# Performance work log

Measured on AMD Instinct MI355X. Metric: run time of the kernel, lower is better.

Reference implementation:

```python
import jax, jax.numpy as jnp
import numpy as np

B, S, H, NH, HD, I = 2, 1024, 4096, 32, 128, 11008
EPS = 1e-6
THETA = 10000.0


def _rmsnorm(x, w):
    v = jnp.mean(x * x, axis=-1, keepdims=True)
    return x * jax.lax.rsqrt(v + EPS) * w


def _quant(x):
    # per-tensor symmetric int8 quantization (scale already folded upstream)
    return jnp.clip(jnp.round(x), -128.0, 127.0)


def _lin_i8(xq_i8, w_i8, scale, bias):
    acc = jnp.matmul(xq_i8.astype(jnp.int32), w_i8.astype(jnp.int32).T)
    return acc.astype(jnp.float32) * scale + bias


def _rope(q, k):
    pos = jnp.arange(S, dtype=jnp.float32)
    inv = 1.0 / (THETA ** (jnp.arange(0, HD, 2, dtype=jnp.float32) / HD))
    f = pos[:, None] * inv[None, :]              # [S, HD/2]
    emb = jnp.concatenate([f, f], axis=-1)        # [S, HD]
    cos = jnp.cos(emb)[None, None]                # [1,1,S,HD]
    sin = jnp.sin(emb)[None, None]
    def rot(x):
        return jnp.concatenate([-x[..., HD // 2:], x[..., :HD // 2]], axis=-1)
    return q * cos + rot(q) * sin, k * cos + rot(k) * sin


def setup_inputs() -> dict:
    key = jax.random.key(0)
    ks = jax.random.split(key, 30)
    def w8(k, o, i):
        return jax.random.randint(k, (o, i), -128, 128, dtype=jnp.int8)
    def sc(k):
        return jax.random.uniform(k, (), jnp.float32, 0.001, 0.01)
    return {
        "hidden_states": jax.random.normal(ks[0], (B, S, H), jnp.float32),
        "ln1_w": jax.random.uniform(ks[1], (H,), jnp.float32, 0.5, 1.5) * 20.0,
        "ln2_w": jax.random.uniform(ks[2], (H,), jnp.float32, 0.5, 1.5) * 20.0,
        "Wq": w8(ks[3], H, H), "Wk": w8(ks[4], H, H), "Wv": w8(ks[5], H, H),
        "Wo": w8(ks[6], H, H),
        "Wg": w8(ks[7], I, H), "Wu": w8(ks[8], I, H), "Wd": w8(ks[9], H, I),
        "bq": jax.random.normal(ks[10], (H,), jnp.float32) * 0.01,
        "bk": jax.random.normal(ks[11], (H,), jnp.float32) * 0.01,
        "bv": jax.random.normal(ks[12], (H,), jnp.float32) * 0.01,
        "bo": jax.random.normal(ks[13], (H,), jnp.float32) * 0.01,
        "bg": jax.random.normal(ks[14], (I,), jnp.float32) * 0.01,
        "bu": jax.random.normal(ks[15], (I,), jnp.float32) * 0.01,
        "bd": jax.random.normal(ks[16], (H,), jnp.float32) * 0.01,
        "sq": sc(ks[17]) * 1e-3, "sk": sc(ks[18]) * 1e-3, "sv": sc(ks[19]) * 1e-3,
        "so": sc(ks[20]) * 1e-3, "sg": sc(ks[21]) * 1e-3, "su": sc(ks[22]) * 1e-3,
        "sd": sc(ks[23]) * 1e-3,
        "o_in_scale": sc(ks[24]), "down_in_scale": sc(ks[25]),
    }


def reference(hidden_states, ln1_w, ln2_w, Wq, Wk, Wv, Wo, Wg, Wu, Wd,
              bq, bk, bv, bo, bg, bu, bd,
              sq, sk, sv, so, sg, su, sd, o_in_scale, down_in_scale):
    residual = hidden_states
    # input RMSNorm (quant scale folded into ln1_w) -> int8 activation
    hq = _quant(_rmsnorm(hidden_states, ln1_w)).astype(jnp.int8)
    q = _lin_i8(hq, Wq, sq, bq).reshape(B, S, NH, HD).transpose(0, 2, 1, 3)
    k = _lin_i8(hq, Wk, sk, bk).reshape(B, S, NH, HD).transpose(0, 2, 1, 3)
    v = _lin_i8(hq, Wv, sv, bv).reshape(B, S, NH, HD).transpose(0, 2, 1, 3)
    q, k = _rope(q, k)
    scores = jnp.einsum("bhqd,bhkd->bhqk", q, k) / np.float32(np.sqrt(HD))
    causal = jnp.tril(jnp.ones((S, S), dtype=bool))
    scores = jnp.where(causal[None, None], scores, jnp.float32(-1e30))
    attn = jax.nn.softmax(scores, axis=-1)
    o = jnp.einsum("bhqk,bhkd->bhqd", attn, v).transpose(0, 2, 1, 3).reshape(B, S, H)
    # o_proj with quant scale (W8A8BFP32OFP32LinearWithQuantScale)
    oq = _quant(o / o_in_scale).astype(jnp.int8)
    h = residual + _lin_i8(oq, Wo, so, bo)
    residual = h
    # post-attention RMSNorm (fc1 quant scale folded into ln2_w)
    hq2 = _quant(_rmsnorm(h, ln2_w)).astype(jnp.int8)
    g = _lin_i8(hq2, Wg, sg, bg)
    u = _lin_i8(hq2, Wu, su, bu)
    a = jax.nn.silu(g) * u
    aq = _quant(a / down_in_scale).astype(jnp.int8)
    out = residual + _lin_i8(aq, Wd, sd, bd)
    return out
```

## Files before the change

kernel.cpp:

```cpp
#include <hip/hip_runtime.h>
#include <math.h>

#define B_  2
#define S_  1024
#define H_  4096
#define NH_ 32
#define HD_ 128
#define I_  11008
#define R_  2048

typedef __attribute__((ext_vector_type(4))) int i32x4;
typedef __attribute__((ext_vector_type(4))) float f32x4;
typedef __attribute__((ext_vector_type(8))) short bf16x8;


__device__ __forceinline__ void gload_lds16(const void* g, void* l) {
    __builtin_amdgcn_global_load_lds(
        (const __attribute__((address_space(1))) unsigned int*)g,
        (__attribute__((address_space(3))) unsigned int*)l, 16, 0, 0);
}

__device__ __forceinline__ unsigned short f2bf(float f) {
    unsigned int u = __float_as_uint(f);
    u += 0x7fffu + ((u >> 16) & 1u);
    return (unsigned short)(u >> 16);
}

__global__ __launch_bounds__(256)
void packW_k(const int* __restrict__ W, signed char* __restrict__ out, const int K)
{
    const int kt = blockIdx.x, cb = blockIdx.y, nk = gridDim.x;
    const int t = threadIdx.x;
    int* otile = (int*)(out + ((long)(cb * nk + kt) << 13));
#pragma unroll
    for (int i = 0; i < 8; ++i) {
        const int o = i * 256 + t;
        const int g = o >> 9, r = (o >> 2) & 127, jj = o & 3;
        const int4 w4 = *(const int4*)(W + (long)(cb * 128 + r) * K + kt * 64 + g * 16 + jj * 4);
        otile[o] = (w4.x & 255) | ((w4.y & 255) << 8) | ((w4.z & 255) << 16) | (w4.w << 24);
    }
}

__global__ __launch_bounds__(256)
void rmsnorm_quant_k(const float* __restrict__ x, const float* __restrict__ w,
                     signed char* __restrict__ out)
{
    __shared__ float red[4];
    const int tid = threadIdx.x;
    const long row = blockIdx.x;
    const float4* xr = (const float4*)(x + row * H_);
    float4 xv[4];
    float ss = 0.f;
#pragma unroll
    for (int i = 0; i < 4; ++i) {
        xv[i] = xr[tid + i * 256];
        ss += xv[i].x * xv[i].x + xv[i].y * xv[i].y
            + xv[i].z * xv[i].z + xv[i].w * xv[i].w;
    }
#pragma unroll
    for (int off = 32; off; off >>= 1) ss += __shfl_xor(ss, off);
    if ((tid & 63) == 0) red[tid >> 6] = ss;
    __syncthreads();
    const float tot = red[0] + red[1] + red[2] + red[3];
    const float sc = 1.f / sqrtf(tot * (1.f / (float)H_) + 1e-6f);
    const float4* wr = (const float4*)w;
    int* ob = (int*)out;
    const long rb = row >> 7;
    const int rr = (int)(row & 127);
#pragma unroll
    for (int i = 0; i < 4; ++i) {
        const float4 wv = wr[tid + i * 256];
        const int b0 = (int)fminf(fmaxf(rintf(xv[i].x * sc * wv.x), -128.f), 127.f);
        const int b1 = (int)fminf(fmaxf(rintf(xv[i].y * sc * wv.y), -128.f), 127.f);
        const int b2 = (int)fminf(fmaxf(rintf(xv[i].z * sc * wv.z), -128.f), 127.f);
        const int b3 = (int)fminf(fmaxf(rintf(xv[i].w * sc * wv.w), -128.f), 127.f);
        const int packed = (b0 & 255) | ((b1 & 255) << 8) | ((b2 & 255) << 16) | (b3 << 24);
        const int j4 = tid + i * 256;
        const long a32 = ((rb * 64 + (j4 >> 4)) << 11) + (((j4 >> 2) & 3) << 9)
                       + (rr << 2) + (j4 & 3);
        ob[a32] = packed;
    }
}

template<int MODE>
__global__ __launch_bounds__(256, 2)
void gemm_i8t(const signed char* __restrict__ A8, const signed char* __restrict__ W8,
              const float* __restrict__ scale_ptr, const float* __restrict__ bias,
              const float* __restrict__ residual, float* __restrict__ C,
              const int N, const int K, const int gx)
{
    __shared__ __align__(16) signed char lsA[2][16384];
    __shared__ __align__(16) signed char lsB[2][16384];

    int bid = blockIdx.x;
    {
        const int nwg = gridDim.x;
        const int q = nwg >> 3, r = nwg & 7;
        const int xcd = bid & 7, idx = bid >> 3;
        bid = (xcd < r) ? (xcd * (q + 1) + idx)
                        : (r * (q + 1) + (xcd - r) * q + idx);
    }
    const int bx = bid % gx, by = bid / gx;

    const int tid  = threadIdx.x;
    const int lane = tid & 63, wid = tid >> 6;
    const int bm = bx << 7, bn = by << 7;
    const int wm = (wid >> 1) << 6, wn = (wid & 1) << 6;

    i32x4 acc[4][4];
#pragma unroll
    for (int m = 0; m < 4; ++m)
#pragma unroll
        for (int n = 0; n < 4; ++n) acc[m][n] = (i32x4){0, 0, 0, 0};

    const int nk  = K >> 6;
    const int nk2 = K >> 7;
    const signed char* abase = A8 + ((long)bx * nk << 13);
    const signed char* bbase = W8 + ((long)by * nk << 13);
    const int sgg = wid * 4096 + lane * 16;
    const int sgl = wid * 4096;

#pragma unroll
    for (int c = 0; c < 4; ++c) {
        gload_lds16(abase + sgg + c * 1024, lsA[0] + sgl + c * 1024);
        gload_lds16(bbase + sgg + c * 1024, lsB[0] + sgl + c * 1024);
    }

    for (int kt = 0; kt < nk2; ++kt) {
        const int cur = kt & 1, nxt = cur ^ 1;
        if (kt + 1 < nk2) {
            const signed char* at = abase + ((long)(kt + 1) << 14);
            const signed char* bt = bbase + ((long)(kt + 1) << 14);
#pragma unroll
            for (int c = 0; c < 4; ++c) {
                gload_lds16(at + sgg + c * 1024, lsA[nxt] + sgl + c * 1024);
                gload_lds16(bt + sgg + c * 1024, lsB[nxt] + sgl + c * 1024);
            }
            asm volatile("s_waitcnt vmcnt(8)" ::: "memory");
        } else {
            asm volatile("s_waitcnt vmcnt(0)" ::: "memory");
        }
        __builtin_amdgcn_s_barrier();

        const int kg = (lane >> 4) * 2048, fr = (lane & 15) * 16;
#pragma unroll
        for (int s = 0; s < 2; ++s) {
            const int off = s * 8192;
            i32x4 af[4], bf[4];
#pragma unroll
            for (int m = 0; m < 4; ++m)
                af[m] = *(const i32x4*)(lsA[cur] + off + kg + wm * 16 + m * 256 + fr);
#pragma unroll
            for (int n = 0; n < 4; ++n)
                bf[n] = *(const i32x4*)(lsB[cur] + off + kg + wn * 16 + n * 256 + fr);
            __builtin_amdgcn_s_setprio(1);
#pragma unroll
            for (int m = 0; m < 4; ++m)
#pragma unroll
                for (int n = 0; n < 4; ++n)
                    acc[m][n] = __builtin_amdgcn_mfma_i32_16x16x64_i8(af[m], bf[n], acc[m][n], 0, 0, 0);
            __builtin_amdgcn_s_setprio(0);
        }
        __builtin_amdgcn_s_barrier();
    }

    const float s = *scale_ptr;
    const int rq = (lane >> 4) * 4, fc = lane & 15;
#pragma unroll
    for (int m = 0; m < 4; ++m) {
#pragma unroll
        for (int n = 0; n < 4; ++n) {
            const int col = bn + wn + n * 16 + fc;
            const float bcol = bias[col];
#pragma unroll
            for (int r = 0; r < 4; ++r) {
                const int row = bm + wm + m * 16 + rq + r;
                float v = (float)acc[m][n][r] * s + bcol;
                if (residual) v += residual[(long)row * N + col];
                C[(long)row * N + col] = v;
            }
        }
    }
}

__global__ __launch_bounds__(256, 2)
void gemm_gu(const signed char* __restrict__ A8, const signed char* __restrict__ G8,
             const signed char* __restrict__ U8,
             const float* __restrict__ sg_p, const float* __restrict__ bg,
             const float* __restrict__ su_p, const float* __restrict__ bu,
             const float* __restrict__ qscale, signed char* __restrict__ out8,
             const int N, const int K, const int gx)
{
    __shared__ __align__(16) signed char lsA[2][8192];
    __shared__ __align__(16) signed char lsG[2][8192];
    __shared__ __align__(16) signed char lsU[2][8192];

    int bid = blockIdx.x;
    {
        const int nwg = gridDim.x;
        const int q = nwg >> 3, r = nwg & 7;
        const int xcd = bid & 7, idx = bid >> 3;
        bid = (xcd < r) ? (xcd * (q + 1) + idx)
                        : (r * (q + 1) + (xcd - r) * q + idx);
    }
    const int bx = bid % gx, by = bid / gx;
    const int tid = threadIdx.x, lane = tid & 63, wid = tid >> 6;
    const int bm = bx << 7, bn = by << 7;
    const int wm = (wid >> 1) << 6, wn = (wid & 1) << 6;

    i32x4 ag[4][4], au[4][4];
#pragma unroll
    for (int m = 0; m < 4; ++m)
#pragma unroll
        for (int n = 0; n < 4; ++n) {
            ag[m][n] = (i32x4){0, 0, 0, 0};
            au[m][n] = (i32x4){0, 0, 0, 0};
        }

    const int nk = K >> 6;
    const signed char* abase = A8 + ((long)bx * nk << 13);
    const signed char* gbase = G8 + ((long)by * nk << 13);
    const signed char* ubase = U8 + ((long)by * nk << 13);
    const int sgg = wid * 2048 + lane * 16;
    const int sgl = wid * 2048;

#pragma unroll
    for (int c = 0; c < 2; ++c) {
        gload_lds16(abase + sgg + c * 1024, lsA[0] + sgl + c * 1024);
        gload_lds16(gbase + sgg + c * 1024, lsG[0] + sgl + c * 1024);
        gload_lds16(ubase + sgg + c * 1024, lsU[0] + sgl + c * 1024);
    }

    for (int kt = 0; kt < nk; ++kt) {
        const int cur = kt & 1, nxt = cur ^ 1;
        if (kt + 1 < nk) {
            const signed char* at = abase + ((long)(kt + 1) << 13);
            const signed char* gt = gbase + ((long)(kt + 1) << 13);
            const signed char* ut = ubase + ((long)(kt + 1) << 13);
#pragma unroll
            for (int c = 0; c < 2; ++c) {
                gload_lds16(at + sgg + c * 1024, lsA[nxt] + sgl + c * 1024);
                gload_lds16(gt + sgg + c * 1024, lsG[nxt] + sgl + c * 1024);
                gload_lds16(ut + sgg + c * 1024, lsU[nxt] + sgl + c * 1024);
            }
            asm volatile("s_waitcnt vmcnt(6)" ::: "memory");
        } else {
            asm volatile("s_waitcnt vmcnt(0)" ::: "memory");
        }
        __builtin_amdgcn_s_barrier();

        const int kg = (lane >> 4) * 2048, fr = (lane & 15) * 16;
        i32x4 af[4], gf[4], uf[4];
#pragma unroll
        for (int m = 0; m < 4; ++m)
            af[m] = *(const i32x4*)(lsA[cur] + kg + wm * 16 + m * 256 + fr);
#pragma unroll
        for (int n = 0; n < 4; ++n) {
            gf[n] = *(const i32x4*)(lsG[cur] + kg + wn * 16 + n * 256 + fr);
            uf[n] = *(const i32x4*)(lsU[cur] + kg + wn * 16 + n * 256 + fr);
        }
        __builtin_amdgcn_s_setprio(1);
#pragma unroll
        for (int m = 0; m < 4; ++m)
#pragma unroll
            for (int n = 0; n < 4; ++n) {
                ag[m][n] = __builtin_amdgcn_mfma_i32_16x16x64_i8(af[m], gf[n], ag[m][n], 0, 0, 0);
                au[m][n] = __builtin_amdgcn_mfma_i32_16x16x64_i8(af[m], uf[n], au[m][n], 0, 0, 0);
            }
        __builtin_amdgcn_s_setprio(0);
        __builtin_amdgcn_s_barrier();
    }

    const float sg = *sg_p, su = *su_p;
    const float dinv = 1.f / qscale[0];
    const int nko = N >> 6;
    const int rq = (lane >> 4) * 4, fc = lane & 15;
#pragma unroll
    for (int m = 0; m < 4; ++m) {
#pragma unroll
        for (int n = 0; n < 4; ++n) {
            const int col = bn + wn + n * 16 + fc;
            const float bgc = bg[col], buc = bu[col];
            const int ktc = col >> 6, kgc = (col >> 4) & 3, jc = col & 15;
#pragma unroll
            for (int r = 0; r < 4; ++r) {
                const int row = bm + wm + m * 16 + rq + r;
                const float g = (float)ag[m][n][r] * sg + bgc;
                const float u = (float)au[m][n][r] * su + buc;
                const float a = g / (1.f + __expf(-g)) * u;
                const float qv = fminf(fmaxf(rintf(a * dinv), -128.f), 127.f);
                const long addr = (((long)(row >> 7) * nko + ktc) << 13)
                                + (kgc << 11) + ((row & 127) << 4) + jc;
                out8[addr] = (signed char)(int)qv;
            }
        }
    }
}

__global__ __launch_bounds__(256)
void rope_k(float* __restrict__ q, float* __restrict__ k)
{
    const int row = blockIdx.x;
    const int s = row & (S_ - 1);
    float* qr = q + (long)row * H_;
    float* kr = k + (long)row * H_;
    for (int t = threadIdx.x; t < NH_ * 64; t += 256) {
        const int nh = t >> 6, i = t & 63;
        const float inv = powf(10000.f, -(float)(2 * i) * (1.f / 128.f));
        const float f = (float)s * inv;
        float sn, c;
        sincosf(f, &sn, &c);
        const int base = nh * 128 + i;
        const float q0 = qr[base], q1 = qr[base + 64];
        qr[base]      = q0 * c - q1 * sn;
        qr[base + 64] = q1 * c + q0 * sn;
        const float k0 = kr[base], k1 = kr[base + 64];
        kr[base]      = k0 * c - k1 * sn;
        kr[base + 64] = k1 * c + k0 * sn;
    }
}

__global__ __launch_bounds__(256, 3)
void attn_mfma_k(const float* __restrict__ q, const float* __restrict__ k,
                 const float* __restrict__ v, signed char* __restrict__ out8,
                 const float* __restrict__ osc)
{
    __shared__ __align__(16) char lsK[8192];
    __shared__ __align__(16) char lsV[10240];
    __shared__ __align__(16) char lsP[4][1024];

    const int tid = threadIdx.x, lane = tid & 63, wid = tid >> 6;
    const int bid = blockIdx.x;
    const int qt = 15 - (bid >> 6);
    const int bh = bid & 63;
    const int b = bh >> 5, h = bh & 31;
    const int q0 = qt * 64;
    const int qw = q0 + wid * 16;

    const float* qbase = q + (long)(b * S_) * H_ + (long)h * HD_;
    const float* kbase = k + (long)(b * S_) * H_ + (long)h * HD_;
    const float* vbase = v + (long)(b * S_) * H_ + (long)h * HD_;

    const int frow = lane & 15, fgrp = lane >> 4;
    const float sc = 0.08838834764831845f;

    bf16x8 qf[4];
    {
        const float* qr = qbase + (long)(qw + frow) * H_;
#pragma unroll
        for (int c = 0; c < 4; ++c) {
            const float4 a = *(const float4*)(qr + c * 32 + fgrp * 8);
            const float4 bq = *(const float4*)(qr + c * 32 + fgrp * 8 + 4);
            bf16x8 t;
            t[0] = (short)f2bf(a.x * sc);  t[1] = (short)f2bf(a.y * sc);
            t[2] = (short)f2bf(a.z * sc);  t[3] = (short)f2bf(a.w * sc);
            t[4] = (short)f2bf(bq.x * sc); t[5] = (short)f2bf(bq.y * sc);
            t[6] = (short)f2bf(bq.z * sc); t[7] = (short)f2bf(bq.w * sc);
            qf[c] = t;
        }
    }

    f32x4 oacc[8];
#pragma unroll
    for (int n2 = 0; n2 < 8; ++n2) oacc[n2] = (f32x4){0.f, 0.f, 0.f, 0.f};
    float mr[4] = {-1e30f, -1e30f, -1e30f, -1e30f};
    float lr[4] = {0.f, 0.f, 0.f, 0.f};

    const int nt = (q0 >> 5) + 2;
    for (int kt = 0; kt < nt; ++kt) {
        if (kt) __syncthreads();
        {
            const float* kg = kbase + (long)(kt * 32) * H_;
            const float* vg = vbase + (long)(kt * 32) * H_;
#pragma unroll
            for (int i = 0; i < 4; ++i) {
                const int lin = i * 256 + tid;
                const int kr = lin >> 5;
                const int d4 = (lin & 31) * 4;
                const float4 kv = *(const float4*)(kg + (long)kr * H_ + d4);
                const float4 vv = *(const float4*)(vg + (long)kr * H_ + d4);
                ushort4 kb;
                kb.x = f2bf(kv.x); kb.y = f2bf(kv.y); kb.z = f2bf(kv.z); kb.w = f2bf(kv.w);
                *(ushort4*)(lsK + kr * 256 + ((d4 * 2) ^ ((kr & 7) << 4))) = kb;
                *(unsigned short*)(lsV + (d4 + 0) * 80 + kr * 2) = f2bf(vv.x);
                *(unsigned short*)(lsV + (d4 + 1) * 80 + kr * 2) = f2bf(vv.y);
                *(unsigned short*)(lsV + (d4 + 2) * 80 + kr * 2) = f2bf(vv.z);
                *(unsigned short*)(lsV + (d4 + 3) * 80 + kr * 2) = f2bf(vv.w);
            }
        }
        __syncthreads();

        if (kt * 32 <= qw + 15) {
            f32x4 s0 = (f32x4){0.f, 0.f, 0.f, 0.f};
            f32x4 s1 = (f32x4){0.f, 0.f, 0.f, 0.f};
            const int swz = (frow & 7) << 4;
#pragma unroll
            for (int c = 0; c < 4; ++c) {
                const int dby = c * 64 + fgrp * 16;
                const bf16x8 kfA = *(const bf16x8*)(lsK + frow * 256 + (dby ^ swz));
                const bf16x8 kfB = *(const bf16x8*)(lsK + (frow + 16) * 256 + (dby ^ swz));
                s0 = __builtin_amdgcn_mfma_f32_16x16x32_bf16(qf[c], kfA, s0, 0, 0, 0);
                s1 = __builtin_amdgcn_mfma_f32_16x16x32_bf16(qf[c], kfB, s1, 0, 0, 0);
            }

            const int colg0 = kt * 32 + frow;
            float cf[4];
#pragma unroll
            for (int r = 0; r < 4; ++r) {
                const int rowg = qw + fgrp * 4 + r;
                const float a0 = (colg0 <= rowg) ? s0[r] : -1e30f;
                const float a1 = (colg0 + 16 <= rowg) ? s1[r] : -1e30f;
                float mx = fmaxf(a0, a1);
#pragma unroll
                for (int off2 = 1; off2 < 16; off2 <<= 1) mx = fmaxf(mx, __shfl_xor(mx, off2));
                const float mnew = fmaxf(mr[r], mx);
                cf[r] = __expf(mr[r] - mnew);
                mr[r] = mnew;
                const float p0 = __expf(a0 - mnew);
                const float p1 = __expf(a1 - mnew);
                float sm = p0 + p1;
#pragma unroll
                for (int off2 = 1; off2 < 16; off2 <<= 1) sm += __shfl_xor(sm, off2);
                lr[r] = lr[r] * cf[r] + sm;
                const int row = fgrp * 4 + r;
                const int psw = (row & 3) << 4;
                *(unsigned short*)(lsP[wid] + row * 64 + ((frow * 2) ^ psw)) = f2bf(p0);
                *(unsigned short*)(lsP[wid] + row * 64 + (((16 + frow) * 2) ^ psw)) = f2bf(p1);
            }
#pragma unroll
            for (int n2 = 0; n2 < 8; ++n2) {
#pragma unroll
                for (int r = 0; r < 4; ++r) oacc[n2][r] *= cf[r];
            }
            const bf16x8 pf = *(const bf16x8*)(lsP[wid] + frow * 64 + ((fgrp * 16) ^ ((frow & 3) << 4)));
#pragma unroll
            for (int n2 = 0; n2 < 8; ++n2) {
                const bf16x8 vf = *(const bf16x8*)(lsV + (n2 * 16 + frow) * 80 + fgrp * 16);
                oacc[n2] = __builtin_amdgcn_mfma_f32_16x16x32_bf16(pf, vf, oacc[n2], 0, 0, 0);
            }
        }
    }

    const float oinv = 1.f / osc[0];
    float inv[4];
#pragma unroll
    for (int r = 0; r < 4; ++r) inv[r] = 1.f / lr[r];
#pragma unroll
    for (int n2 = 0; n2 < 8; ++n2) {
        const int kk = h * 128 + n2 * 16 + frow;
        const int ktc = kk >> 6, kgc = (kk >> 4) & 3, jc = kk & 15;
#pragma unroll
        for (int r = 0; r < 4; ++r) {
            const int rowt = b * S_ + qw + fgrp * 4 + r;
            const float ov = oacc[n2][r] * inv[r];
            const float qv = fminf(fmaxf(rintf(ov * oinv), -128.f), 127.f);
            const long addr = (((long)(rowt >> 7) * 64 + ktc) << 13)
                            + (kgc << 11) + ((rowt & 127) << 4) + jc;
            out8[addr] = (signed char)(int)qv;
        }
    }
}

extern "C" void kernel_launch(void* const* d_in, const int* in_sizes, int n_in,
                              void* d_out, int out_size, void* d_ws, size_t ws_size,
                              hipStream_t stream)
{
    const float* hidden = (const float*)d_in[0];
    const float* ln1 = (const float*)d_in[1];
    const float* ln2 = (const float*)d_in[2];
    const int* Wq = (const int*)d_in[3];
    const int* Wk = (const int*)d_in[4];
    const int* Wv = (const int*)d_in[5];
    const int* Wo = (const int*)d_in[6];
    const int* Wg = (const int*)d_in[7];
    const int* Wu = (const int*)d_in[8];
    const int* Wd = (const int*)d_in[9];
    const float* bq = (const float*)d_in[10];
    const float* bk = (const float*)d_in[11];
    const float* bv = (const float*)d_in[12];
    const float* bo = (const float*)d_in[13];
    const float* bg = (const float*)d_in[14];
    const float* bu = (const float*)d_in[15];
    const float* bd = (const float*)d_in[16];
    const float* sq = (const float*)d_in[17];
    const float* sk = (const float*)d_in[18];
    const float* sv = (const float*)d_in[19];
    const float* so = (const float*)d_in[20];
    const float* sg = (const float*)d_in[21];
    const float* su = (const float*)d_in[22];
    const float* sd = (const float*)d_in[23];
    const float* o_sc = (const float*)d_in[24];
    const float* d_sc = (const float*)d_in[25];

    char* ws = (char*)d_ws;
    signed char* HQ8 = (signed char*)ws;
    signed char* WP  = (signed char*)(ws + ((size_t)22 << 20));
    float* Qb = (float*)(ws + ((size_t)66 << 20));
    float* Kb = (float*)(ws + ((size_t)98 << 20));
    float* Vb = (float*)(ws + ((size_t)130 << 20));
    signed char* WPu = (signed char*)(ws + ((size_t)98 << 20));
    signed char* AQ8 = (signed char*)(ws + ((size_t)184 << 20));
    float* Hb = Qb;
    float* out = (float*)d_out;

    const dim3 blk(256);
    const int gxH = R_ / 128;
    const int nwgH = gxH * (H_ / 128);
    const int nwgI = gxH * (I_ / 128);
    const dim3 gpH(H_ / 64, H_ / 128);
    const dim3 gpI(H_ / 64, I_ / 128);
    const dim3 gpD(I_ / 64, H_ / 128);

    rmsnorm_quant_k<<<R_, blk, 0, stream>>>(hidden, ln1, HQ8);

    packW_k<<<gpH, blk, 0, stream>>>(Wq, WP, H_);
    gemm_i8t<0><<<nwgH, blk, 0, stream>>>(HQ8, WP, sq, bq, nullptr, Qb, H_, H_, gxH);
    packW_k<<<gpH, blk, 0, stream>>>(Wk, WP, H_);
    gemm_i8t<0><<<nwgH, blk, 0, stream>>>(HQ8, WP, sk, bk, nullptr, Kb, H_, H_, gxH);
    packW_k<<<gpH, blk, 0, stream>>>(Wv, WP, H_);
    gemm_i8t<0><<<nwgH, blk, 0, stream>>>(HQ8, WP, sv, bv, nullptr, Vb, H_, H_, gxH);

    rope_k<<<R_, blk, 0, stream>>>(Qb, Kb);
    attn_mfma_k<<<B_ * NH_ * (S_ / 64), blk, 0, stream>>>(Qb, Kb, Vb, HQ8, o_sc);

    packW_k<<<gpH, blk, 0, stream>>>(Wo, WP, H_);
    gemm_i8t<0><<<nwgH, blk, 0, stream>>>(HQ8, WP, so, bo, hidden, Hb, H_, H_, gxH);

    rmsnorm_quant_k<<<R_, blk, 0, stream>>>(Hb, ln2, HQ8);

    packW_k<<<gpI, blk, 0, stream>>>(Wg, WP, H_);
    packW_k<<<gpI, blk, 0, stream>>>(Wu, WPu, H_);
    gemm_gu<<<nwgI, blk, 0, stream>>>(HQ8, WP, WPu, sg, bg, su, bu,
                                      d_sc, AQ8, I_, H_, gxH);
    packW_k<<<gpD, blk, 0, stream>>>(Wd, WP, I_);
    gemm_i8t<0><<<nwgH, blk, 0, stream>>>(AQ8, WP, sd, bd, Hb, out, H_, I_, gxH);
}
```

Baseline: 932.3 us.

## Overlap weight packing with other kernels via extra pack-role workgroups

Replaces the standalone packW_k launches with extra workgroups added to rmsnorm, rope, attention and gate/up GEMM kernels. These workgroups pack the next layer's weights into double-buffered workspace regions. This hides the packing passes behind concurrent compute and cuts the number of kernel launches. The risk is that pack blocks compete for bandwidth and CUs, and that the reshuffled workspace layout must avoid aliasing, for example WPd sharing space with Kb after attention has finished.

Result: slower. 966.8 us (+3.7%).

```diff
diff --git a/kernel.cpp b/kernel.cpp
--- a/kernel.cpp
+++ b/kernel.cpp
@@ -14,6 +14,13 @@
 typedef __attribute__((ext_vector_type(8))) short bf16x8;
 
 
+struct PackJob {
+    const int* W;
+    signed char* out;
+    int nk;
+    int nt;
+};
+
 __device__ __forceinline__ void gload_lds16(const void* g, void* l) {
     __builtin_amdgcn_global_load_lds(
         (const __attribute__((address_space(1))) unsigned int*)g,
@@ -26,27 +33,51 @@
     return (unsigned short)(u >> 16);
 }
 
+__device__ __forceinline__ void pack_tile(const PackJob& j, int t, int tid) {
+    const int nk = j.nk, K = nk << 6;
+    const int kt = t % nk, cb = t / nk;
+    int* otile = (int*)(j.out + ((long)t << 13));
+#pragma unroll
+    for (int i = 0; i < 8; ++i) {
+        const int o = i * 256 + tid;
+        const int g = o >> 9, r = (o >> 2) & 127, jj = o & 3;
+        const int4 w4 = *(const int4*)(j.W + (long)(cb * 128 + r) * K
+                                           + (long)kt * 64 + g * 16 + jj * 4);
+        otile[o] = (w4.x & 255) | ((w4.y & 255) << 8) | ((w4.z & 255) << 16) | (w4.w << 24);
+    }
+}
+
+__device__ __forceinline__ void pack_role3(const PackJob& j1, const PackJob& j2,
+                                           const PackJob& j3, int pb, int np, int tid) {
+    const int tot = j1.nt + j2.nt + j3.nt;
+    for (int t = pb; t < tot; t += np) {
+        int lt = t;
+        if (lt < j1.nt) { pack_tile(j1, lt, tid); continue; }
+        lt -= j1.nt;
+        if (lt < j2.nt) { pack_tile(j2, lt, tid); continue; }
+        pack_tile(j3, lt - j2.nt, tid);
+    }
+}
+
 __global__ __launch_bounds__(256)
 void packW_k(const int* __restrict__ W, signed char* __restrict__ out, const int K)
 {
     const int kt = blockIdx.x, cb = blockIdx.y, nk = gridDim.x;
-    const int t = threadIdx.x;
-    int* otile = (int*)(out + ((long)(cb * nk + kt) << 13));
-#pragma unroll
-    for (int i = 0; i < 8; ++i) {
-        const int o = i * 256 + t;
-        const int g = o >> 9, r = (o >> 2) & 127, jj = o & 3;
-        const int4 w4 = *(const int4*)(W + (long)(cb * 128 + r) * K + kt * 64 + g * 16 + jj * 4);
-        otile[o] = (w4.x & 255) | ((w4.y & 255) << 8) | ((w4.z & 255) << 16) | (w4.w << 24);
-    }
+    PackJob j{W, out, nk, 0};
+    pack_tile(j, cb * nk + kt, threadIdx.x);
 }
 
 __global__ __launch_bounds__(256)
 void rmsnorm_quant_k(const float* __restrict__ x, const float* __restrict__ w,
-                     signed char* __restrict__ out)
-{
+                     signed char* __restrict__ out, PackJob pj)
+{
+    const int tid = threadIdx.x;
+    if (blockIdx.x >= R_) {
+        pack_role3(pj, PackJob{nullptr, nullptr, 0, 0}, PackJob{nullptr, nullptr, 0, 0},
+                   blockIdx.x - R_, gridDim.x - R_, tid);
+        return;
+    }
     __shared__ float red[4];
-    const int tid = threadIdx.x;
     const long row = blockIdx.x;
     const float4* xr = (const float4*)(x + row * H_);
     float4 xv[4];
@@ -82,7 +113,6 @@
     }
 }
 
-template<int MODE>
 __global__ __launch_bounds__(256, 2)
 void gemm_i8t(const signed char* __restrict__ A8, const signed char* __restrict__ W8,
               const float* __restrict__ scale_ptr, const float* __restrict__ bias,
@@ -189,15 +219,20 @@
              const float* __restrict__ sg_p, const float* __restrict__ bg,
              const float* __restrict__ su_p, const float* __restrict__ bu,
              const float* __restrict__ qscale, signed char* __restrict__ out8,
-             const int N, const int K, const int gx)
+             const int N, const int K, const int gx, const int nwgG, PackJob pj)
 {
     __shared__ __align__(16) signed char lsA[2][8192];
     __shared__ __align__(16) signed char lsG[2][8192];
     __shared__ __align__(16) signed char lsU[2][8192];
 
     int bid = blockIdx.x;
+    if (bid >= nwgG) {
+        pack_role3(pj, PackJob{nullptr, nullptr, 0, 0}, PackJob{nullptr, nullptr, 0, 0},
+                   bid - nwgG, gridDim.x - nwgG, threadIdx.x);
+        return;
+    }
     {
-        const int nwg = gridDim.x;
+        const int nwg = nwgG;
         const int q = nwg >> 3, r = nwg & 7;
         const int xcd = bid & 7, idx = bid >> 3;
         bid = (xcd < r) ? (xcd * (q + 1) + idx)
@@ -298,8 +333,13 @@
 }
 
 __global__ __launch_bounds__(256)
-void rope_k(float* __restrict__ q, float* __restrict__ k)
-{
+void rope_k(float* __restrict__ q, float* __restrict__ k, PackJob pj)
+{
+    if (blockIdx.x >= R_) {
+        pack_role3(pj, PackJob{nullptr, nullptr, 0, 0}, PackJob{nullptr, nullptr, 0, 0},
+                   blockIdx.x - R_, gridDim.x - R_, threadIdx.x);
+        return;
+    }
     const int row = blockIdx.x;
     const int s = row & (S_ - 1);
     float* qr = q + (long)row * H_;
@@ -323,14 +363,19 @@
 __global__ __launch_bounds__(256, 3)
 void attn_mfma_k(const float* __restrict__ q, const float* __restrict__ k,
                  const float* __restrict__ v, signed char* __restrict__ out8,
-                 const float* __restrict__ osc)
+                 const float* __restrict__ osc,
+                 PackJob p1, PackJob p2, PackJob p3, const int npack)
 {
     __shared__ __align__(16) char lsK[8192];
     __shared__ __align__(16) char lsV[10240];
     __shared__ __align__(16) char lsP[4][1024];
 
     const int tid = threadIdx.x, lane = tid & 63, wid = tid >> 6;
-    const int bid = blockIdx.x;
+    if (blockIdx.x < npack) {
+        pack_role3(p1, p2, p3, blockIdx.x, npack, tid);
+        return;
+    }
+    const int bid = blockIdx.x - npack;
     const int qt = 15 - (bid >> 6);
     const int bh = bid & 63;
     const int b = bh >> 5, h = bh & 31;
@@ -494,12 +539,14 @@
 
     char* ws = (char*)d_ws;
     signed char* HQ8 = (signed char*)ws;
-    signed char* WP  = (signed char*)(ws + ((size_t)22 << 20));
-    float* Qb = (float*)(ws + ((size_t)66 << 20));
-    float* Kb = (float*)(ws + ((size_t)98 << 20));
-    float* Vb = (float*)(ws + ((size_t)130 << 20));
-    signed char* WPu = (signed char*)(ws + ((size_t)98 << 20));
-    signed char* AQ8 = (signed char*)(ws + ((size_t)184 << 20));
+    signed char* AQ8 = (signed char*)(ws + ((size_t)8 << 20));
+    signed char* WPa = (signed char*)(ws + ((size_t)30 << 20));
+    float* Qb = (float*)(ws + ((size_t)74 << 20));
+    float* Kb = (float*)(ws + ((size_t)106 << 20));
+    float* Vb = (float*)(ws + ((size_t)138 << 20));
+    signed char* WPb = (signed char*)(ws + ((size_t)170 << 20));
+    signed char* WPu = (signed char*)(ws + ((size_t)186 << 20));
+    signed char* WPd = (signed char*)(ws + ((size_t)106 << 20));
     float* Hb = Qb;
     float* out = (float*)d_out;
 
@@ -507,31 +554,29 @@
     const int gxH = R_ / 128;
     const int nwgH = gxH * (H_ / 128);
     const int nwgI = gxH * (I_ / 128);
-    const dim3 gpH(H_ / 64, H_ / 128);
-    const dim3 gpI(H_ / 64, I_ / 128);
-    const dim3 gpD(I_ / 64, H_ / 128);
-
-    rmsnorm_quant_k<<<R_, blk, 0, stream>>>(hidden, ln1, HQ8);
-
-    packW_k<<<gpH, blk, 0, stream>>>(Wq, WP, H_);
-    gemm_i8t<0><<<nwgH, blk, 0, stream>>>(HQ8, WP, sq, bq, nullptr, Qb, H_, H_, gxH);
-    packW_k<<<gpH, blk, 0, stream>>>(Wk, WP, H_);
-    gemm_i8t<0><<<nwgH, blk, 0, stream>>>(HQ8, WP, sk, bk, nullptr, Kb, H_, H_, gxH);
-    packW_k<<<gpH, blk, 0, stream>>>(Wv, WP, H_);
-    gemm_i8t<0><<<nwgH, blk, 0, stream>>>(HQ8, WP, sv, bv, nullptr, Vb, H_, H_, gxH);
-
-    rope_k<<<R_, blk, 0, stream>>>(Qb, Kb);
-    attn_mfma_k<<<B_ * NH_ * (S_ / 64), blk, 0, stream>>>(Qb, Kb, Vb, HQ8, o_sc);
-
-    packW_k<<<gpH, blk, 0, stream>>>(Wo, WP, H_);
-    gemm_i8t<0><<<nwgH, blk, 0, stream>>>(HQ8, WP, so, bo, hidden, Hb, H_, H_, gxH);
-
-    rmsnorm_quant_k<<<R_, blk, 0, stream>>>(Hb, ln2, HQ8);
-
-    packW_k<<<gpI, blk, 0, stream>>>(Wg, WP, H_);
-    packW_k<<<gpI, blk, 0, stream>>>(Wu, WPu, H_);
-    gemm_gu<<<nwgI, blk, 0, stream>>>(HQ8, WP, WPu, sg, bg, su, bu,
-                                      d_sc, AQ8, I_, H_, gxH);
-    packW_k<<<gpD, blk, 0, stream>>>(Wd, WP, I_);
-    gemm_i8t<0><<<nwgH, blk, 0, stream>>>(AQ8, WP, sd, bd, Hb, out, H_, I_, gxH);
-}
+    const int NPK = 256;
+    const int ntH = (H_ / 64) * (H_ / 128);
+    const int ntI = (H_ / 64) * (I_ / 128);
+    const int ntD = (I_ / 64) * (H_ / 128);
+    const PackJob JK{Wk, WPb, H_ / 64, ntH};
+    const PackJob JV{Wv, WPa, H_ / 64, ntH};
+    const PackJob JO{Wo, WPb, H_ / 64, ntH};
+    const PackJob JG{Wg, WPa, H_ / 64, ntI};
+    const PackJob JU{Wu, WPu, H_ / 64, ntI};
+    const PackJob JD{Wd, WPd, I_ / 64, ntD};
+    const PackJob J0{nullptr, nullptr, 0, 0};
+
+    packW_k<<<dim3(H_ / 64, H_ / 128), blk, 0, stream>>>(Wq, WPa, H_);
+    rmsnorm_quant_k<<<R_ + NPK, blk, 0, stream>>>(hidden, ln1, HQ8, JK);
+    gemm_i8t<<<nwgH, blk, 0, stream>>>(HQ8, WPa, sq, bq, nullptr, Qb, H_, H_, gxH);
+    gemm_i8t<<<nwgH, blk, 0, stream>>>(HQ8, WPb, sk, bk, nullptr, Kb, H_, H_, gxH);
+    rope_k<<<R_ + NPK, blk, 0, stream>>>(Qb, Kb, JV);
+    gemm_i8t<<<nwgH, blk, 0, stream>>>(HQ8, WPa, sv, bv, nullptr, Vb, H_, H_, gxH);
+    attn_mfma_k<<<512 + B_ * NH_ * (S_ / 64), blk, 0, stream>>>(
+        Qb, Kb, Vb, HQ8, o_sc, JO, JG, JU, 512);
+    gemm_i8t<<<nwgH, blk, 0, stream>>>(HQ8, WPb, so, bo, hidden, Hb, H_, H_, gxH);
+    rmsnorm_quant_k<<<R_, blk, 0, stream>>>(Hb, ln2, HQ8, J0);
+    gemm_gu<<<nwgI + NPK, blk, 0, stream>>>(HQ8, WPa, WPu, sg, bg, su, bu,
+                                            d_sc, AQ8, I_, H_, gxH, nwgI, JD);
+    gemm_i8t<<<nwgH, blk, 0, stream>>>(AQ8, WPd, sd, bd, Hb, out, H_, I_, gxH);
+}
```
